# Kernel tuning notes

Measured on AMD Instinct MI355X. Metric: run time of the kernel, lower is better.

The kernel has to match this reference:

```python
import jax, jax.numpy as jnp
import numpy as np

EPS_NORM = 1e-12  # F.normalize eps
EPS_BN = 1e-5     # BatchNorm eps


def setup_inputs() -> dict:
    key = jax.random.key(0)
    ks = jax.random.split(key, 8)
    B, N, P, d = 64, 4, 128, 256  # batch, subgraphs, patches/subgraph, feature_dim
    h = 256                        # hidden2[-1]
    C = 2                          # num_class
    totP = N * P                   # 512 == num_patches
    feat = totP * h                # readout size = 131072

    def w(k, shape, s=0.02):
        return jax.random.normal(k, shape, dtype=jnp.float32) * s

    return {
        "x": jax.random.normal(ks[0], (B, totP, d), dtype=jnp.float32),
        "edge_prior_mask": jax.random.uniform(ks[1], (P, P), dtype=jnp.float32),
        # stage1 GCN layers (Linear stored as [in, out])
        "W1": w(ks[2], (d, h)), "b1": jnp.zeros((h,), jnp.float32),
        "g1": jnp.ones((h,), jnp.float32), "be1": jnp.zeros((h,), jnp.float32),
        "W2": w(ks[3], (h, h)), "b2": jnp.zeros((h,), jnp.float32),
        "g2": jnp.ones((h,), jnp.float32), "be2": jnp.zeros((h,), jnp.float32),
        # mlp_causal
        "Wm1": w(ks[4], (feat, 128), 0.005), "bm1": jnp.zeros((128,), jnp.float32),
        "gm1": jnp.ones((128,), jnp.float32), "bem1": jnp.zeros((128,), jnp.float32),
        "Wm2": w(ks[5], (128, 64)), "bm2": jnp.zeros((64,), jnp.float32),
        "gm2": jnp.ones((64,), jnp.float32), "bem2": jnp.zeros((64,), jnp.float32),
        "Wm3": w(ks[6], (64, C)), "bm3": jnp.zeros((C,), jnp.float32),
    }


def reference(x, edge_prior_mask, W1, b1, g1, be1, W2, b2, g2, be2,
              Wm1, bm1, gm1, bem1, Wm2, bm2, gm2, bem2, Wm3, bm3):
    B, totP, d = x.shape
    P = edge_prior_mask.shape[0]
    N = totP // P

    # ---- dynamic edges: per-subgraph cosine similarity * prior mask ----
    xb = x.reshape(B, N, P, d)
    nrm = jnp.linalg.norm(xb, axis=-1, keepdims=True)
    xn = xb / jnp.maximum(nrm, EPS_NORM)
    sim = (jnp.einsum('bnpd,bnqd->bnpq', xn, xn) + 1.0) * 0.5  # [B,N,P,P]
    blocks = sim * edge_prior_mask[None, None]

    # block-diagonal assembly [B, totP, totP]
    edges = jnp.zeros((B, totP, totP), dtype=x.dtype)
    for i in range(N):
        edges = edges.at[:, i * P:(i + 1) * P, i * P:(i + 1) * P].set(blocks[:, i])
    eye = jnp.eye(totP, dtype=x.dtype)
    edges = edges * (1.0 - eye)  # zero the diagonal

    # ---- symmetric degree normalization with self loops ----
    A = edges + eye
    deg = A.sum(-1)  # [B, totP]
    dinv = jnp.where(deg > 0, 1.0 / jnp.sqrt(jnp.maximum(deg, EPS_NORM)), 0.0)
    An = dinv[:, :, None] * A * dinv[:, None, :]

    # ---- two GCN layers: bmm(An, X @ W + b) -> BN (over batch+nodes) -> relu ----
    def bn_relu(hh, g, b):
        m = hh.mean(axis=(0, 1), keepdims=True)
        v = hh.var(axis=(0, 1), keepdims=True)
        return jax.nn.relu(g * (hh - m) / jnp.sqrt(v + EPS_BN) + b)

    h1 = bn_relu(jnp.einsum('bpq,bqh->bph', An, x @ W1 + b1), g1, be1)
    h2 = bn_relu(jnp.einsum('bpq,bqh->bph', An, h1 @ W2 + b2), g2, be2)

    # ---- readout + MLP head (dropout = identity in eval) ----
    graph = h2.reshape(B, -1)

    def bn1d(z, g, b):
        m = z.mean(0, keepdims=True)
        v = z.var(0, keepdims=True)
        return g * (z - m) / jnp.sqrt(v + EPS_BN) + b

    z = jax.nn.relu(bn1d(graph @ Wm1 + bm1, gm1, bem1))
    z = jax.nn.relu(bn1d(z @ Wm2 + bm2, gm2, bem2))
    return z @ Wm3 + bm3
```

## Files before the change

### kernel.cpp

```cpp
#include <hip/hip_runtime.h>
#include <cstdint>
#include <cstddef>

#define P_    128
#define H_    256
#define FEAT_ 131072

#define SIM_XS   0
#define SIM_RED  2048
#define SIM_DIAG 4224
#define SIM_INV  4352
#define SIM_DINV 4480
#define GE_AS    0
#define GE_WS    2112

__global__ __launch_bounds__(256) void k_simgemm(
    const float* __restrict__ x, const float* __restrict__ mask,
    float* __restrict__ An,
    const float* __restrict__ W, const float* __restrict__ bias,
    float* __restrict__ out) {
  __shared__ float smem[4608];
  const int bid = blockIdx.x;
  const int t = threadIdx.x, tp = t >> 4, tq = t & 15;

  if (bid < 256) {
    const int blk = bid;
    const float* Xb = x + (size_t)blk * (128 * 256);

    float v[8][8];
    #pragma unroll
    for (int i = 0; i < 8; ++i)
      #pragma unroll
      for (int j = 0; j < 8; ++j) v[i][j] = 0.f;

    for (int kc = 0; kc < 16; ++kc) {
      __syncthreads();
      #pragma unroll
      for (int l = 0; l < 2; ++l) {
        const int f = t + 256 * l;
        const int row = f >> 2, k4 = (f & 3) * 4;
        const float4 x4 = *(const float4*)(Xb + (size_t)row * 256 + kc * 16 + k4);
        smem[SIM_XS + (k4 + 0) * 128 + row] = x4.x;
        smem[SIM_XS + (k4 + 1) * 128 + row] = x4.y;
        smem[SIM_XS + (k4 + 2) * 128 + row] = x4.z;
        smem[SIM_XS + (k4 + 3) * 128 + row] = x4.w;
      }
      __syncthreads();
      #pragma unroll
      for (int k = 0; k < 16; ++k) {
        const float4 a0 = *(const float4*)&smem[SIM_XS + k * 128 + tp * 8];
        const float4 a1 = *(const float4*)&smem[SIM_XS + k * 128 + tp * 8 + 4];
        const float4 b0 = *(const float4*)&smem[SIM_XS + k * 128 + tq * 8];
        const float4 b1 = *(const float4*)&smem[SIM_XS + k * 128 + tq * 8 + 4];
        const float a[8] = {a0.x, a0.y, a0.z, a0.w, a1.x, a1.y, a1.z, a1.w};
        const float b[8] = {b0.x, b0.y, b0.z, b0.w, b1.x, b1.y, b1.z, b1.w};
        #pragma unroll
        for (int i = 0; i < 8; ++i)
          #pragma unroll
          for (int j = 0; j < 8; ++j) v[i][j] += a[i] * b[j];
      }
    }

    if (tp == tq) {
      #pragma unroll
      for (int i = 0; i < 8; ++i) smem[SIM_DIAG + tp * 8 + i] = v[i][i];
    }
    __syncthreads();
    if (t < 128)
      smem[SIM_INV + t] = 1.0f / fmaxf(sqrtf(smem[SIM_DIAG + t]), 1e-12f);
    __syncthreads();

    float ivq[8];
    #pragma unroll
    for (int j = 0; j < 8; ++j) ivq[j] = smem[SIM_INV + tq * 8 + j];

    #pragma unroll
    for (int i = 0; i < 8; ++i) {
      const int r = tp * 8 + i;
      const float ivp = smem[SIM_INV + r];
      const float4 m0 = *(const float4*)(mask + r * 128 + tq * 8);
      const float4 m1 = *(const float4*)(mask + r * 128 + tq * 8 + 4);
      const float mm[8] = {m0.x, m0.y, m0.z, m0.w, m1.x, m1.y, m1.z, m1.w};
      float s = 0.f;
      #pragma unroll
      for (int j = 0; j < 8; ++j) {
        const int c = tq * 8 + j;
        const float vv = (r == c) ? 0.0f
                                  : (v[i][j] * ivp * ivq[j] + 1.0f) * 0.5f * mm[j];
        v[i][j] = vv;
        s += vv;
      }
      smem[SIM_RED + r * 17 + tq] = s;
    }
    __syncthreads();
    if (t < 128) {
      float sm = 0.f;
      #pragma unroll
      for (int u = 0; u < 16; ++u) sm += smem[SIM_RED + t * 17 + u];
      const float deg = 1.0f + sm;
      smem[SIM_DINV + t] = (deg > 0.0f) ? rsqrtf(fmaxf(deg, 1e-12f)) : 0.0f;
    }
    __syncthreads();

    float dq[8];
    #pragma unroll
    for (int j = 0; j < 8; ++j) dq[j] = smem[SIM_DINV + tq * 8 + j];
    float* Ab = An + (size_t)blk * 16384;
    #pragma unroll
    for (int i = 0; i < 8; ++i) {
      const int r = tp * 8 + i;
      const float dp = smem[SIM_DINV + r];
      float o[8];
      #pragma unroll
      for (int j = 0; j < 8; ++j) {
        const int c = tq * 8 + j;
        o[j] = (r == c) ? dp * dq[j] : v[i][j] * dp * dq[j];
      }
      *(float4*)(Ab + (size_t)r * 128 + tq * 8)     = make_float4(o[0], o[1], o[2], o[3]);
      *(float4*)(Ab + (size_t)r * 128 + tq * 8 + 4) = make_float4(o[4], o[5], o[6], o[7]);
    }
  } else {
    const int g = bid - 256;
    const int rb = g >> 1, cb = g & 1;
    const int m0 = rb * 128, c0 = cb * 128;

    float acc[8][8];
    #pragma unroll
    for (int j = 0; j < 8; ++j) {
      const int cj = (j < 4) ? (tq * 4 + j) : (64 + tq * 4 + (j - 4));
      const float bj = bias[c0 + cj];
      #pragma unroll
      for (int i = 0; i < 8; ++i) acc[i][j] = bj;
    }

    for (int kc = 0; kc < 16; ++kc) {
      __syncthreads();
      #pragma unroll
      for (int l = 0; l < 2; ++l) {
        const int f = t + 256 * l;
        const int row = f >> 2, k4 = (f & 3) * 4;
        const float4 a4 = *(const float4*)(x + (size_t)(m0 + row) * 256 + kc * 16 + k4);
        smem[GE_AS + (k4 + 0) * 132 + row] = a4.x;
        smem[GE_AS + (k4 + 1) * 132 + row] = a4.y;
        smem[GE_AS + (k4 + 2) * 132 + row] = a4.z;
        smem[GE_AS + (k4 + 3) * 132 + row] = a4.w;
      }
      #pragma unroll
      for (int l = 0; l < 2; ++l) {
        const int f = t + 256 * l;
        const int k = f >> 5, c4 = (f & 31) * 4;
        *(float4*)&smem[GE_WS + k * 132 + c4] =
            *(const float4*)(W + (size_t)(kc * 16 + k) * 256 + c0 + c4);
      }
      __syncthreads();
      #pragma unroll
      for (int k = 0; k < 16; ++k) {
        const float4 a0 = *(const float4*)&smem[GE_AS + k * 132 + tp * 4];
        const float4 a1 = *(const float4*)&smem[GE_AS + k * 132 + 64 + tp * 4];
        const float4 w0 = *(const float4*)&smem[GE_WS + k * 132 + tq * 4];
        const float4 w1 = *(const float4*)&smem[GE_WS + k * 132 + 64 + tq * 4];
        const float a[8] = {a0.x, a0.y, a0.z, a0.w, a1.x, a1.y, a1.z, a1.w};
        const float w[8] = {w0.x, w0.y, w0.z, w0.w, w1.x, w1.y, w1.z, w1.w};
        #pragma unroll
        for (int i = 0; i < 8; ++i)
          #pragma unroll
          for (int j = 0; j < 8; ++j) acc[i][j] += a[i] * w[j];
      }
    }

    #pragma unroll
    for (int i = 0; i < 8; ++i) {
      const int ri = (i < 4) ? (tp * 4 + i) : (64 + tp * 4 + (i - 4));
      float* orow = out + (size_t)(m0 + ri) * 256 + c0;
      *(float4*)(orow + tq * 4)      = make_float4(acc[i][0], acc[i][1], acc[i][2], acc[i][3]);
      *(float4*)(orow + 64 + tq * 4) = make_float4(acc[i][4], acc[i][5], acc[i][6], acc[i][7]);
    }
  }
}

__global__ __launch_bounds__(256) void k_gemmbn_t(
    const float* __restrict__ A, const float* __restrict__ scsh,
    const float* __restrict__ W, const float* __restrict__ bias,
    float* __restrict__ out) {
  __shared__ float As[16][132];
  __shared__ float Ws[16][132];
  const int rb = blockIdx.x, cb = blockIdx.y;
  const int t = threadIdx.x, tp = t >> 4, tq = t & 15;
  const int m0 = rb * 128, c0 = cb * 128;

  float acc[8][8];
  #pragma unroll
  for (int j = 0; j < 8; ++j) {
    const int cj = (j < 4) ? (tq * 4 + j) : (64 + tq * 4 + (j - 4));
    const float bj = bias[c0 + cj];
    #pragma unroll
    for (int i = 0; i < 8; ++i) acc[i][j] = bj;
  }

  for (int kc = 0; kc < 16; ++kc) {
    __syncthreads();
    #pragma unroll
    for (int l = 0; l < 2; ++l) {
      const int f = t + 256 * l;
      const int row = f >> 2, k4 = (f & 3) * 4;
      const int col = kc * 16 + k4;
      const float4 a4 = *(const float4*)(A + (size_t)(m0 + row) * 256 + col);
      const float4 sc = *(const float4*)(scsh + col);
      const float4 sh = *(const float4*)(scsh + 256 + col);
      As[k4 + 0][row] = fmaxf(a4.x * sc.x + sh.x, 0.0f);
      As[k4 + 1][row] = fmaxf(a4.y * sc.y + sh.y, 0.0f);
      As[k4 + 2][row] = fmaxf(a4.z * sc.z + sh.z, 0.0f);
      As[k4 + 3][row] = fmaxf(a4.w * sc.w + sh.w, 0.0f);
    }
    #pragma unroll
    for (int l = 0; l < 2; ++l) {
      const int f = t + 256 * l;
      const int k = f >> 5, c4 = (f & 31) * 4;
      *(float4*)&Ws[k][c4] =
          *(const float4*)(W + (size_t)(kc * 16 + k) * 256 + c0 + c4);
    }
    __syncthreads();
    #pragma unroll
    for (int k = 0; k < 16; ++k) {
      const float4 a0 = *(const float4*)&As[k][tp * 4];
      const float4 a1 = *(const float4*)&As[k][64 + tp * 4];
      const float4 w0 = *(const float4*)&Ws[k][tq * 4];
      const float4 w1 = *(const float4*)&Ws[k][64 + tq * 4];
      const float a[8] = {a0.x, a0.y, a0.z, a0.w, a1.x, a1.y, a1.z, a1.w};
      const float w[8] = {w0.x, w0.y, w0.z, w0.w, w1.x, w1.y, w1.z, w1.w};
      #pragma unroll
      for (int i = 0; i < 8; ++i)
        #pragma unroll
        for (int j = 0; j < 8; ++j) acc[i][j] += a[i] * w[j];
    }
  }

  #pragma unroll
  for (int i = 0; i < 8; ++i) {
    const int ri = (i < 4) ? (tp * 4 + i) : (64 + tp * 4 + (i - 4));
    float* orow = out + (size_t)(m0 + ri) * 256 + c0;
    *(float4*)(orow + tq * 4)      = make_float4(acc[i][0], acc[i][1], acc[i][2], acc[i][3]);
    *(float4*)(orow + 64 + tq * 4) = make_float4(acc[i][4], acc[i][5], acc[i][6], acc[i][7]);
  }
}

__global__ __launch_bounds__(256) void k_bmmst(
    const float* __restrict__ An, const float* __restrict__ XW,
    float* __restrict__ out, float* __restrict__ part) {
  __shared__ float As[16][132];
  __shared__ float Ws[16][132];
  __shared__ float rs[16][128];
  __shared__ float rq[16][128];
  const int blk = blockIdx.x, cb = blockIdx.y;
  const int t = threadIdx.x, tp = t >> 4, tq = t & 15;
  const float* Ab = An + (size_t)blk * 16384;
  const float* Xb = XW + (size_t)blk * (128 * 256);

  float acc[8][8];
  #pragma unroll
  for (int i = 0; i < 8; ++i)
    #pragma unroll
    for (int j = 0; j < 8; ++j) acc[i][j] = 0.f;

  for (int kc = 0; kc < 8; ++kc) {
    __syncthreads();
    #pragma unroll
    for (int l = 0; l < 2; ++l) {
      const int f = t + 256 * l;
      const int row = f >> 2, k4 = (f & 3) * 4;
      const float4 a4 = *(const float4*)(Ab + (size_t)row * 128 + kc * 16 + k4);
      As[k4 + 0][row] = a4.x;
      As[k4 + 1][row] = a4.y;
      As[k4 + 2][row] = a4.z;
      As[k4 + 3][row] = a4.w;
    }
    #pragma unroll
    for (int l = 0; l < 2; ++l) {
      const int f = t + 256 * l;
      const int k = f >> 5, c4 = (f & 31) * 4;
      *(float4*)&Ws[k][c4] =
          *(const float4*)(Xb + (size_t)(kc * 16 + k) * 256 + cb * 128 + c4);
    }
    __syncthreads();
    #pragma unroll
    for (int k = 0; k < 16; ++k) {
      const float4 a0 = *(const float4*)&As[k][tp * 4];
      const float4 a1 = *(const float4*)&As[k][64 + tp * 4];
      const float4 w0 = *(const float4*)&Ws[k][tq * 4];
      const float4 w1 = *(const float4*)&Ws[k][64 + tq * 4];
      const float a[8] = {a0.x, a0.y, a0.z, a0.w, a1.x, a1.y, a1.z, a1.w};
      const float w[8] = {w0.x, w0.y, w0.z, w0.w, w1.x, w1.y, w1.z, w1.w};
      #pragma unroll
      for (int i = 0; i < 8; ++i)
        #pragma unroll
        for (int j = 0; j < 8; ++j) acc[i][j] += a[i] * w[j];
    }
  }

  #pragma unroll
  for (int j = 0; j < 8; ++j) {
    const int col = (j < 4) ? (tq * 4 + j) : (64 + tq * 4 + (j - 4));
    float cs = 0.f, cq = 0.f;
    #pragma unroll
    for (int i = 0; i < 8; ++i) { cs += acc[i][j]; cq += acc[i][j] * acc[i][j]; }
    rs[tp][col] = cs;
    rq[tp][col] = cq;
  }
  __syncthreads();
  if (t < 128) {
    float s = 0.f, q = 0.f;
    #pragma unroll
    for (int u = 0; u < 16; ++u) { s += rs[u][t]; q += rq[u][t]; }
    const int base = (blk * 2 + cb) * 256;
    part[base + t]       = s;
    part[base + 128 + t] = q;
  }

  #pragma unroll
  for (int i = 0; i < 8; ++i) {
    const int ri = (i < 4) ? (tp * 4 + i) : (64 + tp * 4 + (i - 4));
    float* orow = out + (size_t)(blk * 128 + ri) * 256 + cb * 128;
    *(float4*)(orow + tq * 4)      = make_float4(acc[i][0], acc[i][1], acc[i][2], acc[i][3]);
    *(float4*)(orow + 64 + tq * 4) = make_float4(acc[i][4], acc[i][5], acc[i][6], acc[i][7]);
  }
}

__global__ __launch_bounds__(256) void k_bnscsh(
    const float* __restrict__ part, const float* __restrict__ g,
    const float* __restrict__ be, float* __restrict__ scsh) {
  __shared__ float ss[256], qq[256];
  const int c = blockIdx.x;
  const int cb = c >> 7, lc = c & 127;
  const int u = threadIdx.x;
  const float* pb = part + (size_t)(u * 2 + cb) * 256;
  ss[u] = pb[lc];
  qq[u] = pb[128 + lc];
  __syncthreads();
  for (int st = 128; st; st >>= 1) {
    if (u < st) { ss[u] += ss[u + st]; qq[u] += qq[u + st]; }
    __syncthreads();
  }
  if (u == 0) {
    const float m = ss[0] * (1.0f / 32768.0f);
    const float var = qq[0] * (1.0f / 32768.0f) - m * m;
    const float sc = g[c] * rsqrtf(var + 1e-5f);
    scsh[c] = sc;
    scsh[256 + c] = be[c] - m * sc;
  }
}

__global__ __launch_bounds__(256) void k_headgemm_v3(
    const float* __restrict__ pre2, const float* __restrict__ scsh,
    const float* __restrict__ Wm1, float* __restrict__ part) {
  __shared__ float graphS[64][128];
  const int t = threadIdx.x;
  const int bid = blockIdx.x;
  const int k0 = bid * 128;
  const int cbase = k0 & 255;

  #pragma unroll
  for (int l = 0; l < 8; ++l) {
    const int f = t + 256 * l;
    const int row = f >> 5, c4 = (f & 31) * 4;
    const float4 p = *(const float4*)(pre2 + (size_t)row * FEAT_ + k0 + c4);
    const float4 sc = *(const float4*)(scsh + cbase + c4);
    const float4 sh = *(const float4*)(scsh + 256 + cbase + c4);
    graphS[row][c4 + 0] = fmaxf(p.x * sc.x + sh.x, 0.0f);
    graphS[row][c4 + 1] = fmaxf(p.y * sc.y + sh.y, 0.0f);
    graphS[row][c4 + 2] = fmaxf(p.z * sc.z + sh.z, 0.0f);
    graphS[row][c4 + 3] = fmaxf(p.w * sc.w + sh.w, 0.0f);
  }
  __syncthreads();

  const int hg = t & 31;
  const int bg = t >> 5;
  float acc[8][4];
  #pragma unroll
  for (int i = 0; i < 8; ++i)
    #pragma unroll
    for (int j = 0; j < 4; ++j) acc[i][j] = 0.f;

  #pragma unroll 2
  for (int kk = 0; kk < 128; kk += 4) {
    const int k = k0 + kk;
    const float4 w0 = *(const float4*)(Wm1 + (size_t)(k + 0) * 128 + hg * 4);
    const float4 w1 = *(const float4*)(Wm1 + (size_t)(k + 1) * 128 + hg * 4);
    const float4 w2 = *(const float4*)(Wm1 + (size_t)(k + 2) * 128 + hg * 4);
    const float4 w3 = *(const float4*)(Wm1 + (size_t)(k + 3) * 128 + hg * 4);
    #pragma unroll
    for (int i = 0; i < 8; ++i) {
      const float4 a = *(const float4*)&graphS[bg * 8 + i][kk];
      acc[i][0] += a.x * w0.x; acc[i][1] += a.x * w0.y;
      acc[i][2] += a.x * w0.z; acc[i][3] += a.x * w0.w;
      acc[i][0] += a.y * w1.x; acc[i][1] += a.y * w1.y;
      acc[i][2] += a.y * w1.z; acc[i][3] += a.y * w1.w;
      acc[i][0] += a.z * w2.x; acc[i][1] += a.z * w2.y;
      acc[i][2] += a.z * w2.z; acc[i][3] += a.z * w2.w;
      acc[i][0] += a.w * w3.x; acc[i][1] += a.w * w3.y;
      acc[i][2] += a.w * w3.z; acc[i][3] += a.w * w3.w;
    }
  }

  float* pb = part + (size_t)bid * 8192;
  #pragma unroll
  for (int i = 0; i < 8; ++i)
    *(float4*)(pb + (bg * 8 + i) * 128 + hg * 4) =
        make_float4(acc[i][0], acc[i][1], acc[i][2], acc[i][3]);
}

__global__ __launch_bounds__(256) void k_headredA(
    const float* __restrict__ part, float* __restrict__ part2) {
  const int o = blockIdx.x * 256 + threadIdx.x;
  const int jg = blockIdx.y;
  const float* base = part + (size_t)jg * 128 * 8192;
  float s = 0.f;
  for (int j = 0; j < 128; ++j) s += base[(size_t)j * 8192 + o];
  part2[(size_t)jg * 8192 + o] = s;
}

__global__ __launch_bounds__(256) void k_headtail(
    const float* __restrict__ part2,
    const float* __restrict__ gm1, const float* __restrict__ bem1,
    const float* __restrict__ Wm2,
    const float* __restrict__ gm2, const float* __restrict__ bem2,
    const float* __restrict__ Wm3, const float* __restrict__ bm3,
    float* __restrict__ out) {
  __shared__ float zs[8192];
  __shared__ float wm2s[8192];
  __shared__ float zb2[4096];
  __shared__ float sc1[128], sh1[128], sc2[64], sh2[64];
  const int t = threadIdx.x;

  for (int o = t; o < 8192; o += 256) {
    float s = 0.f;
    #pragma unroll
    for (int jg = 0; jg < 8; ++jg) s += part2[(size_t)jg * 8192 + o];
    zs[o] = s;
  }
  for (int o = t; o < 8192; o += 256) wm2s[o] = Wm2[o];
  __syncthreads();

  if (t < 128) {
    float s = 0.f, q = 0.f;
    for (int b = 0; b < 64; ++b) { const float v = zs[b * 128 + t]; s += v; q += v * v; }
    const float m = s * (1.0f / 64.0f);
    const float var = q * (1.0f / 64.0f) - m * m;
    const float sc = gm1[t] * rsqrtf(var + 1e-5f);
    sc1[t] = sc; sh1[t] = bem1[t] - m * sc;
  }
  __syncthreads();
  for (int o = t; o < 8192; o += 256)
    zs[o] = fmaxf(zs[o] * sc1[o & 127] + sh1[o & 127], 0.0f);
  __syncthreads();

  {
    const int bq = t >> 4, jq = t & 15;
    float acc[4][4];
    #pragma unroll
    for (int bi = 0; bi < 4; ++bi)
      #pragma unroll
      for (int ji = 0; ji < 4; ++ji) acc[bi][ji] = 0.f;
    for (int k = 0; k < 128; ++k) {
      const float4 w4 = *(const float4*)&wm2s[k * 64 + jq * 4];
      const float wv[4] = {w4.x, w4.y, w4.z, w4.w};
      #pragma unroll
      for (int bi = 0; bi < 4; ++bi) {
        const float zv = zs[(bq * 4 + bi) * 128 + k];
        #pragma unroll
        for (int ji = 0; ji < 4; ++ji) acc[bi][ji] += zv * wv[ji];
      }
    }
    #pragma unroll
    for (int bi = 0; bi < 4; ++bi)
      #pragma unroll
      for (int ji = 0; ji < 4; ++ji)
        zb2[(bq * 4 + bi) * 64 + jq * 4 + ji] = acc[bi][ji];
  }
  __syncthreads();

  if (t < 64) {
    float s = 0.f, q = 0.f;
    for (int b = 0; b < 64; ++b) { const float v = zb2[b * 64 + t]; s += v; q += v * v; }
    const float m = s * (1.0f / 64.0f);
    const float var = q * (1.0f / 64.0f) - m * m;
    const float sc = gm2[t] * rsqrtf(var + 1e-5f);
    sc2[t] = sc; sh2[t] = bem2[t] - m * sc;
  }
  __syncthreads();
  for (int idx = t; idx < 4096; idx += 256)
    zb2[idx] = fmaxf(zb2[idx] * sc2[idx & 63] + sh2[idx & 63], 0.0f);
  __syncthreads();

  if (t < 128) {
    const int b = t >> 1, c = t & 1;
    float s = bm3[c];
    for (int k = 0; k < 64; ++k) s += zb2[b * 64 + k] * Wm3[k * 2 + c];
    out[t] = s;
  }
}

extern "C" void kernel_launch(void* const* d_in, const int* in_sizes, int n_in,
                              void* d_out, int out_size, void* d_ws, size_t ws_size,
                              hipStream_t stream) {
  (void)in_sizes; (void)n_in; (void)out_size; (void)ws_size;
  const float* x    = (const float*)d_in[0];
  const float* mask = (const float*)d_in[1];
  const float* W1   = (const float*)d_in[2];
  const float* b1   = (const float*)d_in[3];
  const float* g1   = (const float*)d_in[4];
  const float* be1  = (const float*)d_in[5];
  const float* W2   = (const float*)d_in[6];
  const float* b2   = (const float*)d_in[7];
  const float* g2   = (const float*)d_in[8];
  const float* be2  = (const float*)d_in[9];
  const float* Wm1  = (const float*)d_in[10];
  const float* gm1  = (const float*)d_in[12];
  const float* bem1 = (const float*)d_in[13];
  const float* Wm2  = (const float*)d_in[14];
  const float* gm2  = (const float*)d_in[16];
  const float* bem2 = (const float*)d_in[17];
  const float* Wm3  = (const float*)d_in[18];
  const float* bm3  = (const float*)d_in[19];

  float* ws   = (float*)d_ws;
  float* T1   = ws;
  float* An   = T1 + 8388608;
  float* T2   = An + 4194304;
  float* T3   = T2 + 8388608;
  float* z1   = T3 + 8388608;
  float* dinv = z1 + 8192;
  (void)z1;

  float* scsh1 = dinv;
  float* scsh2 = dinv + 512;

  k_simgemm<<<768, 256, 0, stream>>>(x, mask, An, W1, b1, T2);

  k_bmmst<<<dim3(256, 2), 256, 0, stream>>>(An, T2, T3, T1);
  k_bnscsh<<<256, 256, 0, stream>>>(T1, g1, be1, scsh1);

  k_gemmbn_t<<<dim3(256, 2), 256, 0, stream>>>(T3, scsh1, W2, b2, T2);
  k_bmmst<<<dim3(256, 2), 256, 0, stream>>>(An, T2, T3, T1);
  k_bnscsh<<<256, 256, 0, stream>>>(T1, g2, be2, scsh2);

  k_headgemm_v3<<<1024, 256, 0, stream>>>(T3, scsh2, Wm1, T2);
  k_headredA<<<dim3(32, 8), 256, 0, stream>>>(T2, An);
  k_headtail<<<1, 256, 0, stream>>>(An, gm1, bem1, Wm2, gm2, bem2,
                                    Wm3, bm3, (float*)d_out);
}
```

Measured before the change: 401.9 us.

## Fuse BN stat reduction into consumers, double-buffer GEMM, pad similarity smem

Removes the two k_bnscsh launches by having each block of k_gemmbn_t and k_headgemm_v3 reduce the per-channel BN partial sums itself before use. k_gemmbn_t gains register-prefetch double buffering of its A/W shared tiles, so each k-step needs one barrier instead of two. The similarity GEMM's shared layout is padded to a stride of 132 and threads take interleaved 4-wide column groups to cut LDS bank conflicts. The cost is redundant reduction work: every one of 512 and 1024 blocks rereads 256 partial rows from global memory, which lengthens each block's prologue.

```diff
diff --git a/kernel.cpp b/kernel.cpp
--- a/kernel.cpp
+++ b/kernel.cpp
@@ -7,10 +7,10 @@
 #define FEAT_ 131072
 
 #define SIM_XS   0
-#define SIM_RED  2048
-#define SIM_DIAG 4224
-#define SIM_INV  4352
-#define SIM_DINV 4480
+#define SIM_RED  2112
+#define SIM_DIAG 4288
+#define SIM_INV  4416
+#define SIM_DINV 4544
 #define GE_AS    0
 #define GE_WS    2112
 
@@ -19,7 +19,7 @@
     float* __restrict__ An,
     const float* __restrict__ W, const float* __restrict__ bias,
     float* __restrict__ out) {
-  __shared__ float smem[4608];
+  __shared__ float smem[4672];
   const int bid = blockIdx.x;
   const int t = threadIdx.x, tp = t >> 4, tq = t & 15;
 
@@ -40,18 +40,18 @@
         const int f = t + 256 * l;
         const int row = f >> 2, k4 = (f & 3) * 4;
         const float4 x4 = *(const float4*)(Xb + (size_t)row * 256 + kc * 16 + k4);
-        smem[SIM_XS + (k4 + 0) * 128 + row] = x4.x;
-        smem[SIM_XS + (k4 + 1) * 128 + row] = x4.y;
-        smem[SIM_XS + (k4 + 2) * 128 + row] = x4.z;
-        smem[SIM_XS + (k4 + 3) * 128 + row] = x4.w;
+        smem[SIM_XS + (k4 + 0) * 132 + row] = x4.x;
+        smem[SIM_XS + (k4 + 1) * 132 + row] = x4.y;
+        smem[SIM_XS + (k4 + 2) * 132 + row] = x4.z;
+        smem[SIM_XS + (k4 + 3) * 132 + row] = x4.w;
       }
       __syncthreads();
       #pragma unroll
       for (int k = 0; k < 16; ++k) {
-        const float4 a0 = *(const float4*)&smem[SIM_XS + k * 128 + tp * 8];
-        const float4 a1 = *(const float4*)&smem[SIM_XS + k * 128 + tp * 8 + 4];
-        const float4 b0 = *(const float4*)&smem[SIM_XS + k * 128 + tq * 8];
-        const float4 b1 = *(const float4*)&smem[SIM_XS + k * 128 + tq * 8 + 4];
+        const float4 a0 = *(const float4*)&smem[SIM_XS + k * 132 + tp * 4];
+        const float4 a1 = *(const float4*)&smem[SIM_XS + k * 132 + 64 + tp * 4];
+        const float4 b0 = *(const float4*)&smem[SIM_XS + k * 132 + tq * 4];
+        const float4 b1 = *(const float4*)&smem[SIM_XS + k * 132 + 64 + tq * 4];
         const float a[8] = {a0.x, a0.y, a0.z, a0.w, a1.x, a1.y, a1.z, a1.w};
         const float b[8] = {b0.x, b0.y, b0.z, b0.w, b1.x, b1.y, b1.z, b1.w};
         #pragma unroll
@@ -63,7 +63,10 @@
 
     if (tp == tq) {
       #pragma unroll
-      for (int i = 0; i < 8; ++i) smem[SIM_DIAG + tp * 8 + i] = v[i][i];
+      for (int i = 0; i < 8; ++i) {
+        const int r = (i < 4) ? (tp * 4 + i) : (64 + tp * 4 + (i - 4));
+        smem[SIM_DIAG + r] = v[i][i];
+      }
     }
     __syncthreads();
     if (t < 128)
@@ -72,19 +75,22 @@
 
     float ivq[8];
     #pragma unroll
-    for (int j = 0; j < 8; ++j) ivq[j] = smem[SIM_INV + tq * 8 + j];
+    for (int j = 0; j < 8; ++j) {
+      const int c = (j < 4) ? (tq * 4 + j) : (64 + tq * 4 + (j - 4));
+      ivq[j] = smem[SIM_INV + c];
+    }
 
     #pragma unroll
     for (int i = 0; i < 8; ++i) {
-      const int r = tp * 8 + i;
+      const int r = (i < 4) ? (tp * 4 + i) : (64 + tp * 4 + (i - 4));
       const float ivp = smem[SIM_INV + r];
-      const float4 m0 = *(const float4*)(mask + r * 128 + tq * 8);
-      const float4 m1 = *(const float4*)(mask + r * 128 + tq * 8 + 4);
+      const float4 m0 = *(const float4*)(mask + r * 128 + tq * 4);
+      const float4 m1 = *(const float4*)(mask + r * 128 + 64 + tq * 4);
       const float mm[8] = {m0.x, m0.y, m0.z, m0.w, m1.x, m1.y, m1.z, m1.w};
       float s = 0.f;
       #pragma unroll
       for (int j = 0; j < 8; ++j) {
-        const int c = tq * 8 + j;
+        const int c = (j < 4) ? (tq * 4 + j) : (64 + tq * 4 + (j - 4));
         const float vv = (r == c) ? 0.0f
                                   : (v[i][j] * ivp * ivq[j] + 1.0f) * 0.5f * mm[j];
         v[i][j] = vv;
@@ -104,20 +110,23 @@
 
     float dq[8];
     #pragma unroll
-    for (int j = 0; j < 8; ++j) dq[j] = smem[SIM_DINV + tq * 8 + j];
+    for (int j = 0; j < 8; ++j) {
+      const int c = (j < 4) ? (tq * 4 + j) : (64 + tq * 4 + (j - 4));
+      dq[j] = smem[SIM_DINV + c];
+    }
     float* Ab = An + (size_t)blk * 16384;
     #pragma unroll
     for (int i = 0; i < 8; ++i) {
-      const int r = tp * 8 + i;
+      const int r = (i < 4) ? (tp * 4 + i) : (64 + tp * 4 + (i - 4));
       const float dp = smem[SIM_DINV + r];
       float o[8];
       #pragma unroll
       for (int j = 0; j < 8; ++j) {
-        const int c = tq * 8 + j;
+        const int c = (j < 4) ? (tq * 4 + j) : (64 + tq * 4 + (j - 4));
         o[j] = (r == c) ? dp * dq[j] : v[i][j] * dp * dq[j];
       }
-      *(float4*)(Ab + (size_t)r * 128 + tq * 8)     = make_float4(o[0], o[1], o[2], o[3]);
-      *(float4*)(Ab + (size_t)r * 128 + tq * 8 + 4) = make_float4(o[4], o[5], o[6], o[7]);
+      *(float4*)(Ab + (size_t)r * 128 + tq * 4)      = make_float4(o[0], o[1], o[2], o[3]);
+      *(float4*)(Ab + (size_t)r * 128 + 64 + tq * 4) = make_float4(o[4], o[5], o[6], o[7]);
     }
   } else {
     const int g = bid - 256;
@@ -179,15 +188,32 @@
 }
 
 __global__ __launch_bounds__(256) void k_gemmbn_t(
-    const float* __restrict__ A, const float* __restrict__ scsh,
+    const float* __restrict__ A, const float* __restrict__ part,
+    const float* __restrict__ g, const float* __restrict__ be,
     const float* __restrict__ W, const float* __restrict__ bias,
     float* __restrict__ out) {
-  __shared__ float As[16][132];
-  __shared__ float Ws[16][132];
+  __shared__ float As[2][16][132];
+  __shared__ float Ws[2][16][132];
+  __shared__ float scsh[512];
   const int rb = blockIdx.x, cb = blockIdx.y;
   const int t = threadIdx.x, tp = t >> 4, tq = t & 15;
   const int m0 = rb * 128, c0 = cb * 128;
 
+  {
+    const int ch = t, hb = ch >> 7, lc = ch & 127;
+    float s = 0.f, q = 0.f;
+    for (int u = 0; u < 256; ++u) {
+      const float* pb = part + (size_t)(u * 2 + hb) * 256;
+      s += pb[lc];
+      q += pb[128 + lc];
+    }
+    const float m = s * (1.0f / 32768.0f);
+    const float var = q * (1.0f / 32768.0f) - m * m;
+    const float sc = g[ch] * rsqrtf(var + 1e-5f);
+    scsh[ch] = sc;
+    scsh[256 + ch] = be[ch] - m * sc;
+  }
+
   float acc[8][8];
   #pragma unroll
   for (int j = 0; j < 8; ++j) {
@@ -197,41 +223,73 @@
     for (int i = 0; i < 8; ++i) acc[i][j] = bj;
   }
 
+  __syncthreads();
+
+  float4 ra[2], rw[2];
+  #pragma unroll
+  for (int l = 0; l < 2; ++l) {
+    const int f = t + 256 * l;
+    const int row = f >> 2, k4 = (f & 3) * 4;
+    ra[l] = *(const float4*)(A + (size_t)(m0 + row) * 256 + k4);
+    const int kk = f >> 5, c4 = (f & 31) * 4;
+    rw[l] = *(const float4*)(W + (size_t)kk * 256 + c0 + c4);
+  }
+  #pragma unroll
+  for (int l = 0; l < 2; ++l) {
+    const int f = t + 256 * l;
+    const int row = f >> 2, k4 = (f & 3) * 4;
+    const float4 sc = *(const float4*)&scsh[k4];
+    const float4 sh = *(const float4*)&scsh[256 + k4];
+    As[0][k4 + 0][row] = fmaxf(ra[l].x * sc.x + sh.x, 0.0f);
+    As[0][k4 + 1][row] = fmaxf(ra[l].y * sc.y + sh.y, 0.0f);
+    As[0][k4 + 2][row] = fmaxf(ra[l].z * sc.z + sh.z, 0.0f);
+    As[0][k4 + 3][row] = fmaxf(ra[l].w * sc.w + sh.w, 0.0f);
+    const int kk = f >> 5, c4 = (f & 31) * 4;
+    *(float4*)&Ws[0][kk][c4] = rw[l];
+  }
+
   for (int kc = 0; kc < 16; ++kc) {
-    __syncthreads();
-    #pragma unroll
-    for (int l = 0; l < 2; ++l) {
-      const int f = t + 256 * l;
-      const int row = f >> 2, k4 = (f & 3) * 4;
-      const int col = kc * 16 + k4;
-      const float4 a4 = *(const float4*)(A + (size_t)(m0 + row) * 256 + col);
-      const float4 sc = *(const float4*)(scsh + col);
-      const float4 sh = *(const float4*)(scsh + 256 + col);
-      As[k4 + 0][row] = fmaxf(a4.x * sc.x + sh.x, 0.0f);
-      As[k4 + 1][row] = fmaxf(a4.y * sc.y + sh.y, 0.0f);
-      As[k4 + 2][row] = fmaxf(a4.z * sc.z + sh.z, 0.0f);
-      As[k4 + 3][row] = fmaxf(a4.w * sc.w + sh.w, 0.0f);
-    }
-    #pragma unroll
-    for (int l = 0; l < 2; ++l) {
-      const int f = t + 256 * l;
-      const int k = f >> 5, c4 = (f & 31) * 4;
-      *(float4*)&Ws[k][c4] =
-          *(const float4*)(W + (size_t)(kc * 16 + k) * 256 + c0 + c4);
+    const int cur = kc & 1;
+    if (kc < 15) {
+      const int kn = (kc + 1) * 16;
+      #pragma unroll
+      for (int l = 0; l < 2; ++l) {
+        const int f = t + 256 * l;
+        const int row = f >> 2, k4 = (f & 3) * 4;
+        ra[l] = *(const float4*)(A + (size_t)(m0 + row) * 256 + kn + k4);
+        const int kk = f >> 5, c4 = (f & 31) * 4;
+        rw[l] = *(const float4*)(W + (size_t)(kn + kk) * 256 + c0 + c4);
+      }
     }
     __syncthreads();
     #pragma unroll
     for (int k = 0; k < 16; ++k) {
-      const float4 a0 = *(const float4*)&As[k][tp * 4];
-      const float4 a1 = *(const float4*)&As[k][64 + tp * 4];
-      const float4 w0 = *(const float4*)&Ws[k][tq * 4];
-      const float4 w1 = *(const float4*)&Ws[k][64 + tq * 4];
+      const float4 a0 = *(const float4*)&As[cur][k][tp * 4];
+      const float4 a1 = *(const float4*)&As[cur][k][64 + tp * 4];
+      const float4 w0 = *(const float4*)&Ws[cur][k][tq * 4];
+      const float4 w1 = *(const float4*)&Ws[cur][k][64 + tq * 4];
       const float a[8] = {a0.x, a0.y, a0.z, a0.w, a1.x, a1.y, a1.z, a1.w};
       const float w[8] = {w0.x, w0.y, w0.z, w0.w, w1.x, w1.y, w1.z, w1.w};
       #pragma unroll
       for (int i = 0; i < 8; ++i)
         #pragma unroll
         for (int j = 0; j < 8; ++j) acc[i][j] += a[i] * w[j];
+    }
+    if (kc < 15) {
+      const int kn = (kc + 1) * 16;
+      #pragma unroll
+      for (int l = 0; l < 2; ++l) {
+        const int f = t + 256 * l;
+        const int row = f >> 2, k4 = (f & 3) * 4;
+        const float4 sc = *(const float4*)&scsh[kn + k4];
+        const float4 sh = *(const float4*)&scsh[256 + kn + k4];
+        As[cur ^ 1][k4 + 0][row] = fmaxf(ra[l].x * sc.x + sh.x, 0.0f);
+        As[cur ^ 1][k4 + 1][row] = fmaxf(ra[l].y * sc.y + sh.y, 0.0f);
+        As[cur ^ 1][k4 + 2][row] = fmaxf(ra[l].z * sc.z + sh.z, 0.0f);
+        As[cur ^ 1][k4 + 3][row] = fmaxf(ra[l].w * sc.w + sh.w, 0.0f);
+        const int kk = f >> 5, c4 = (f & 31) * 4;
+        *(float4*)&Ws[cur ^ 1][kk][c4] = rw[l];
+      }
     }
   }
 
@@ -325,46 +383,40 @@
   }
 }
 
-__global__ __launch_bounds__(256) void k_bnscsh(
-    const float* __restrict__ part, const float* __restrict__ g,
-    const float* __restrict__ be, float* __restrict__ scsh) {
-  __shared__ float ss[256], qq[256];
-  const int c = blockIdx.x;
-  const int cb = c >> 7, lc = c & 127;
-  const int u = threadIdx.x;
-  const float* pb = part + (size_t)(u * 2 + cb) * 256;
-  ss[u] = pb[lc];
-  qq[u] = pb[128 + lc];
-  __syncthreads();
-  for (int st = 128; st; st >>= 1) {
-    if (u < st) { ss[u] += ss[u + st]; qq[u] += qq[u + st]; }
-    __syncthreads();
-  }
-  if (u == 0) {
-    const float m = ss[0] * (1.0f / 32768.0f);
-    const float var = qq[0] * (1.0f / 32768.0f) - m * m;
-    const float sc = g[c] * rsqrtf(var + 1e-5f);
-    scsh[c] = sc;
-    scsh[256 + c] = be[c] - m * sc;
-  }
-}
-
 __global__ __launch_bounds__(256) void k_headgemm_v3(
-    const float* __restrict__ pre2, const float* __restrict__ scsh,
-    const float* __restrict__ Wm1, float* __restrict__ part) {
+    const float* __restrict__ pre2, const float* __restrict__ part,
+    const float* __restrict__ g, const float* __restrict__ be,
+    const float* __restrict__ Wm1, float* __restrict__ partout) {
   __shared__ float graphS[64][128];
+  __shared__ float scshh[256];
   const int t = threadIdx.x;
   const int bid = blockIdx.x;
   const int k0 = bid * 128;
   const int cbase = k0 & 255;
 
+  if (t < 128) {
+    const int ch = cbase + t, hb = ch >> 7, lc = ch & 127;
+    float s = 0.f, q = 0.f;
+    for (int u = 0; u < 256; ++u) {
+      const float* pb = part + (size_t)(u * 2 + hb) * 256;
+      s += pb[lc];
+      q += pb[128 + lc];
+    }
+    const float m = s * (1.0f / 32768.0f);
+    const float var = q * (1.0f / 32768.0f) - m * m;
+    const float sc = g[ch] * rsqrtf(var + 1e-5f);
+    scshh[t] = sc;
+    scshh[128 + t] = be[ch] - m * sc;
+  }
+  __syncthreads();
+
   #pragma unroll
   for (int l = 0; l < 8; ++l) {
     const int f = t + 256 * l;
     const int row = f >> 5, c4 = (f & 31) * 4;
     const float4 p = *(const float4*)(pre2 + (size_t)row * FEAT_ + k0 + c4);
-    const float4 sc = *(const float4*)(scsh + cbase + c4);
-    const float4 sh = *(const float4*)(scsh + 256 + cbase + c4);
+    const float4 sc = *(const float4*)&scshh[c4];
+    const float4 sh = *(const float4*)&scshh[128 + c4];
     graphS[row][c4 + 0] = fmaxf(p.x * sc.x + sh.x, 0.0f);
     graphS[row][c4 + 1] = fmaxf(p.y * sc.y + sh.y, 0.0f);
     graphS[row][c4 + 2] = fmaxf(p.z * sc.z + sh.z, 0.0f);
@@ -401,7 +453,7 @@
     }
   }
 
-  float* pb = part + (size_t)bid * 8192;
+  float* pb = partout + (size_t)bid * 8192;
   #pragma unroll
   for (int i = 0; i < 8; ++i)
     *(float4*)(pb + (bg * 8 + i) * 128 + hg * 4) =
@@ -527,23 +579,15 @@
   float* An   = T1 + 8388608;
   float* T2   = An + 4194304;
   float* T3   = T2 + 8388608;
-  float* z1   = T3 + 8388608;
-  float* dinv = z1 + 8192;
-  (void)z1;
-
-  float* scsh1 = dinv;
-  float* scsh2 = dinv + 512;
 
   k_simgemm<<<768, 256, 0, stream>>>(x, mask, An, W1, b1, T2);
 
   k_bmmst<<<dim3(256, 2), 256, 0, stream>>>(An, T2, T3, T1);
-  k_bnscsh<<<256, 256, 0, stream>>>(T1, g1, be1, scsh1);
-
-  k_gemmbn_t<<<dim3(256, 2), 256, 0, stream>>>(T3, scsh1, W2, b2, T2);
+
+  k_gemmbn_t<<<dim3(256, 2), 256, 0, stream>>>(T3, T1, g1, be1, W2, b2, T2);
   k_bmmst<<<dim3(256, 2), 256, 0, stream>>>(An, T2, T3, T1);
-  k_bnscsh<<<256, 256, 0, stream>>>(T1, g2, be2, scsh2);
-
-  k_headgemm_v3<<<1024, 256, 0, stream>>>(T3, scsh2, Wm1, T2);
+
+  k_headgemm_v3<<<1024, 256, 0, stream>>>(T3, T1, g2, be2, Wm1, T2);
   k_headredA<<<dim3(32, 8), 256, 0, stream>>>(T2, An);
   k_headtail<<<1, 256, 0, stream>>>(An, gm1, bem1, Wm2, gm2, bem2,
                                     Wm3, bm3, (float*)d_out);
```

After: 460.0 us. 14.4% more time.
